# Performance work log

Measured on AMD Instinct MI355X. Metric: run time of the kernel, lower is better.

Reference implementation:

```python
import jax, jax.numpy as jnp
import numpy as np

H = 32        # num_attention_heads
KVH = 8       # num_key_value_heads
D = 64        # head_dim
HID = 2048    # hidden_size
G = H // KVH  # num_key_value_groups


def setup_inputs() -> dict:
    key = jax.random.key(0)
    k1, k2, k3, k4, k5 = jax.random.split(key, 5)
    B, S = 1, 2048
    s = 1.0 / np.sqrt(HID)
    return {
        "hidden_states": jax.random.normal(k1, (B, S, HID), dtype=jnp.float32),
        "attention_mask": jnp.ones((B, S), dtype=jnp.int32),
        "Wq": jax.random.normal(k2, (H * D, HID), dtype=jnp.float32) * s,
        "Wk": jax.random.normal(k3, (KVH * D, HID), dtype=jnp.float32) * s,
        "Wv": jax.random.normal(k4, (KVH * D, HID), dtype=jnp.float32) * s,
        "Wo": jax.random.normal(k5, (HID, HID), dtype=jnp.float32) * s,
    }


def reference(hidden_states, attention_mask, Wq, Wk, Wv, Wo):
    B, S, _ = hidden_states.shape
    dtype = hidden_states.dtype

    q = (hidden_states @ Wq.T).reshape(B, S, H, D).transpose(0, 2, 1, 3)     # [B,H,S,D]
    k = (hidden_states @ Wk.T).reshape(B, S, KVH, D).transpose(0, 2, 1, 3)   # [B,KVH,S,D]
    v = (hidden_states @ Wv.T).reshape(B, S, KVH, D).transpose(0, 2, 1, 3)

    # repeat_interleave over head dim: each KV head serves G query heads
    k = jnp.repeat(k, G, axis=1)  # [B,H,S,D]
    v = jnp.repeat(v, G, axis=1)

    scores = jnp.einsum('bhqd,bhkd->bhqk', q, k) / np.sqrt(D)  # [B,H,S,S]

    causal = jnp.tril(jnp.ones((S, S), dtype=dtype))                # [S,S]
    am = attention_mask.astype(dtype)[:, None, None, :]              # [B,1,1,S]
    mask = am * causal[None, None, :, :]                             # [B,1,S,S]
    mask = (1.0 - mask) * jnp.finfo(dtype).min
    scores = scores + mask                                           # broadcast over heads

    weights = jax.nn.softmax(scores, axis=-1)
    attn = jnp.einsum('bhqk,bhkd->bhqd', weights, v)                 # [B,H,S,D]
    attn = attn.transpose(0, 2, 1, 3).reshape(B, S, HID)
    return attn @ Wo.T
```

## Files before the change

kernel.cpp:

```cpp
#include <hip/hip_runtime.h>
#include <hip/hip_bf16.h>
#include <math.h>

typedef __attribute__((ext_vector_type(4))) float f32x4;
typedef __attribute__((ext_vector_type(16))) float f32x16;
typedef __attribute__((ext_vector_type(8))) short bf16x8;
typedef __attribute__((ext_vector_type(4))) short s16x4;
typedef __attribute__((ext_vector_type(4))) unsigned int u32x4;
typedef __attribute__((ext_vector_type(2))) unsigned int u32x2;
typedef short s16;
typedef unsigned int u32;
typedef unsigned short u16;

#define S_LEN 2048
#define HIDN  2048
#define QKVW  3072
#define NH    32
#define NKVH  8
#define HD    64

__device__ __forceinline__ s16 f2bf(float f) {
  unsigned int u = __float_as_uint(f);
  unsigned int lsb = (u >> 16) & 1u;
  u += 0x7fffu + lsb;
  return (s16)(u >> 16);
}

__device__ __forceinline__ u32 cvtpk(float lo, float hi) {
  u32 r;
  asm("v_cvt_pk_bf16_f32 %0, %1, %2" : "=v"(r) : "v"(lo), "v"(hi));
  return r;
}

__device__ __forceinline__ void gload16(const void* g, void* l) {
  __builtin_amdgcn_global_load_lds(
      (const __attribute__((address_space(1))) void*)g,
      (__attribute__((address_space(3))) void*)l, 16, 0, 0);
}

__device__ __forceinline__ void pls(u32& a, u32& b) {
  asm volatile("v_permlane32_swap_b32 %0, %1" : "+v"(a), "+v"(b));
}

__device__ __forceinline__ int swz7(int row) { return (row ^ (row >> 3)) & 7; }

__global__ __launch_bounds__(256) void cvt_all(const float* __restrict__ h,
                                               const float* __restrict__ wq,
                                               const float* __restrict__ wk,
                                               const float* __restrict__ wv,
                                               const float* __restrict__ wo,
                                               s16x4* __restrict__ dst) {
  int i = blockIdx.x * 256 + threadIdx.x;
  const float* src; int off;
  if (i < 1048576)      { src = h;  off = i; }
  else if (i < 2097152) { src = wq; off = i - 1048576; }
  else if (i < 2359296) { src = wk; off = i - 2097152; }
  else if (i < 2621440) { src = wv; off = i - 2359296; }
  else                  { src = wo; off = i - 2621440; }
  if (i < 3670016) {
    float4 f = reinterpret_cast<const float4*>(src)[off];
    s16x4 o;
    o.x = f2bf(f.x); o.y = f2bf(f.y); o.z = f2bf(f.z); o.w = f2bf(f.w);
    dst[i] = o;
  }
}

__device__ __forceinline__ void storeC(s16* C, size_t idx, float v)   { C[idx] = f2bf(v); }
__device__ __forceinline__ void storeC(float* C, size_t idx, float v) { C[idx] = v; }

template <typename OUT_T>
__global__ __launch_bounds__(512) void gemm_bt(const s16* __restrict__ A,
                                               const s16* __restrict__ B,
                                               OUT_T* __restrict__ C,
                                               int M, int N, int K, int gridX) {
  __shared__ alignas(16) s16 As[2][8192];
  __shared__ alignas(16) s16 Bs[2][8192];

  const int nwg  = (M >> 7) * gridX;
  const int flat = blockIdx.x;
  const int q8   = nwg >> 3;
  const int swz  = (flat & 7) * q8 + (flat >> 3);
  const int bm   = (swz / gridX) * 128;
  const int bn   = (swz % gridX) * 128;

  const int t    = threadIdx.x;
  const int lane = t & 63;
  const int w    = t >> 6;
  const int wr   = (w >> 2) * 64;
  const int wc   = (w & 3) * 32;
  const int lr   = lane & 15;
  const int lg   = lane >> 4;

  const int srow0 = (w * 2) * 8 + (lane >> 3);
  const int srow1 = (w * 2 + 1) * 8 + (lane >> 3);
  const int sl0   = ((lane & 7) ^ swz7(srow0)) * 8;
  const int sl1   = ((lane & 7) ^ swz7(srow1)) * 8;

  f32x4 acc[4][2];
#pragma unroll
  for (int m = 0; m < 4; ++m)
#pragma unroll
    for (int n = 0; n < 2; ++n)
      acc[m][n] = (f32x4){0.f, 0.f, 0.f, 0.f};

  const int nK = K >> 6;
  int buf = 0;

  {
    gload16(&A[(size_t)(bm + srow0) * K + sl0], (char*)As[0] + (w * 2) * 1024);
    gload16(&A[(size_t)(bm + srow1) * K + sl1], (char*)As[0] + (w * 2 + 1) * 1024);
    gload16(&B[(size_t)(bn + srow0) * K + sl0], (char*)Bs[0] + (w * 2) * 1024);
    gload16(&B[(size_t)(bn + srow1) * K + sl1], (char*)Bs[0] + (w * 2 + 1) * 1024);
  }
  __syncthreads();

  for (int ki = 0; ki < nK; ++ki) {
    if (ki + 1 < nK) {
      const int kt = (ki + 1) << 6;
      gload16(&A[(size_t)(bm + srow0) * K + kt + sl0], (char*)As[buf ^ 1] + (w * 2) * 1024);
      gload16(&A[(size_t)(bm + srow1) * K + kt + sl1], (char*)As[buf ^ 1] + (w * 2 + 1) * 1024);
      gload16(&B[(size_t)(bn + srow0) * K + kt + sl0], (char*)Bs[buf ^ 1] + (w * 2) * 1024);
      gload16(&B[(size_t)(bn + srow1) * K + kt + sl1], (char*)Bs[buf ^ 1] + (w * 2 + 1) * 1024);
    }

    bf16x8 af[4][2], bfr[2][2];
#pragma unroll
    for (int kk = 0; kk < 2; ++kk) {
#pragma unroll
      for (int m = 0; m < 4; ++m) {
        int row = wr + m * 16 + lr;
        af[m][kk] = *(bf16x8*)((char*)As[buf] + row * 128 + (((kk * 4 + lg) ^ swz7(row)) << 4));
      }
#pragma unroll
      for (int n = 0; n < 2; ++n) {
        int row = wc + n * 16 + lr;
        bfr[n][kk] = *(bf16x8*)((char*)Bs[buf] + row * 128 + (((kk * 4 + lg) ^ swz7(row)) << 4));
      }
    }

    __builtin_amdgcn_s_setprio(1);
#pragma unroll
    for (int m = 0; m < 4; ++m)
#pragma unroll
      for (int n = 0; n < 2; ++n)
#pragma unroll
        for (int kk = 0; kk < 2; ++kk)
          acc[m][n] = __builtin_amdgcn_mfma_f32_16x16x32_bf16(af[m][kk], bfr[n][kk], acc[m][n], 0, 0, 0);
    __builtin_amdgcn_s_setprio(0);

    __syncthreads();
    buf ^= 1;
  }

#pragma unroll
  for (int m = 0; m < 4; ++m)
#pragma unroll
    for (int n = 0; n < 2; ++n) {
      int row = bm + wr + m * 16 + lg * 4;
      int col = bn + wc + n * 16 + lr;
#pragma unroll
      for (int j = 0; j < 4; ++j)
        storeC(C, (size_t)(row + j) * N + col, acc[m][n][j]);
    }
}

__global__ __launch_bounds__(512) void attn_kernel(
    const s16* __restrict__ QKV,
    const int* __restrict__ am,
    s16* __restrict__ Ob) {
  __shared__ alignas(16) char smem[65536];
  __shared__ float2 mlb[4][64];

  const int t    = threadIdx.x;
  const int g    = t >> 8;
  const int tg   = t & 255;
  const int lane = t & 63;
  const int w    = tg >> 6;
  const int col  = lane & 31;
  const int hi   = lane >> 5;

  const int hk = blockIdx.x;
  const int p  = blockIdx.y;
  const int h  = hk * 4 + w;
  const int kbase = 2048 + hk * 64;
  const int vbase = 2560 + hk * 64;
  const float CF = 0.18033688f;

  const int krow   = lane >> 3;
  const int kslotb = lane & 7;
  const int vkv    = 2 * (tg >> 3);
  const int vd8    = (tg & 7) * 8;

  for (int phase = 0; phase < 2; ++phase) {
    const int qt = phase ? p : 63 - p;
    const int nt = (qt >> 1) + 1;
    const int R  = (nt + 1) >> 1;
    const int qrow = qt * 32 + col;

    bf16x8 qf[4];
#pragma unroll
    for (int ds = 0; ds < 4; ++ds)
      qf[ds] = *(const bf16x8*)&QKV[(size_t)qrow * QKVW + h * 64 + ds * 16 + hi * 8];

    if (g < nt) {
      char* Kn = smem + (g * 2 + 0) * 16384;
      char* Vn = Kn + 8192;
#pragma unroll
      for (int pp = 0; pp < 2; ++pp) {
        int c   = w * 2 + pp;
        int row = c * 8 + krow;
        int slot = kslotb ^ swz7(row);
        gload16(&QKV[(size_t)(g * 64 + row) * QKVW + kbase + slot * 8], Kn + c * 1024);
      }
      bf16x8 va = *(const bf16x8*)&QKV[(size_t)(g * 64 + vkv) * QKVW + vbase + vd8];
      bf16x8 vb = *(const bf16x8*)&QKV[(size_t)(g * 64 + vkv + 1) * QKVW + vbase + vd8];
#pragma unroll
      for (int i = 0; i < 8; ++i) {
        int d = vd8 + i;
        u32 pk = (u32)(u16)va[i] | ((u32)(u16)vb[i] << 16);
        *(u32*)&Vn[(d * 128 + vkv * 2) ^ (swz7(d) << 4)] = pk;
      }
    }
    int acur = am[g * 64 + lane];

    float m_i = -1e30f, l_part = 0.f;
    f32x16 Oacc[2];
#pragma unroll
    for (int b = 0; b < 2; ++b)
#pragma unroll
      for (int i = 0; i < 16; ++i) Oacc[b][i] = 0.f;
    __syncthreads();

    for (int it = 0; it < R; ++it) {
      const int buf  = it & 1;
      const int tile = 2 * it + g;
      const bool valid = (tile < nt);
      const int kv0  = tile * 64;
      const bool pre = (tile + 2 < nt);

      char* Kc = smem + (g * 2 + buf) * 16384;
      char* Vc = Kc + 8192;
      char* Kn = smem + (g * 2 + (buf ^ 1)) * 16384;
      char* Vn = Kn + 8192;

      bf16x8 va, vb;
      int anext = 0;
      if (pre) {
        const int nk0 = kv0 + 128;
#pragma unroll
        for (int pp = 0; pp < 2; ++pp) {
          int c   = w * 2 + pp;
          int row = c * 8 + krow;
          int slot = kslotb ^ swz7(row);
          gload16(&QKV[(size_t)(nk0 + row) * QKVW + kbase + slot * 8], Kn + c * 1024);
        }
        va = *(const bf16x8*)&QKV[(size_t)(nk0 + vkv) * QKVW + vbase + vd8];
        vb = *(const bf16x8*)&QKV[(size_t)(nk0 + vkv + 1) * QKVW + vbase + vd8];
        anext = am[nk0 + lane];
      }

      if (valid) {
        f32x16 s0, s1;
#pragma unroll
        for (int i = 0; i < 16; ++i) { s0[i] = 0.f; s1[i] = 0.f; }
        __builtin_amdgcn_s_setprio(1);
#pragma unroll
        for (int ds = 0; ds < 4; ++ds) {
          int off = ds * 32 + hi * 16;
          bf16x8 k0 = *(bf16x8*)&Kc[(col * 128 + off) ^ (swz7(col) << 4)];
          bf16x8 k1 = *(bf16x8*)&Kc[((32 + col) * 128 + off) ^ (swz7(32 + col) << 4)];
          s0 = __builtin_amdgcn_mfma_f32_32x32x16_bf16(k0, qf[ds], s0, 0, 0, 0);
          s1 = __builtin_amdgcn_mfma_f32_32x32x16_bf16(k1, qf[ds], s1, 0, 0, 0);
        }
        __builtin_amdgcn_s_setprio(0);

        float pvv[32];
        unsigned long long m64 = __ballot(acur != 0);
        bool interior = (kv0 + 64 <= qt * 32) && (m64 == ~0ull);
        if (interior) {
#pragma unroll
          for (int r = 0; r < 16; ++r) { pvv[r] = s0[r]; pvv[16 + r] = s1[r]; }
        } else {
#pragma unroll
          for (int b = 0; b < 2; ++b)
#pragma unroll
            for (int r = 0; r < 16; ++r) {
              int kvl = b * 32 + (r & 3) + 8 * (r >> 2) + 4 * hi;
              float sv = b ? s1[r] : s0[r];
              bool ok = (kv0 + kvl <= qrow) && ((m64 >> kvl) & 1ull);
              pvv[b * 16 + r] = ok ? sv : -INFINITY;
            }
        }

        float a0 = pvv[0], a1 = pvv[1], a2 = pvv[2], a3 = pvv[3];
#pragma unroll
        for (int i = 4; i < 32; i += 4) {
          a0 = fmaxf(a0, pvv[i]);     a1 = fmaxf(a1, pvv[i + 1]);
          a2 = fmaxf(a2, pvv[i + 2]); a3 = fmaxf(a3, pvv[i + 3]);
        }
        float lmax = fmaxf(fmaxf(a0, a1), fmaxf(a2, a3));
        lmax = fmaxf(lmax, __shfl_xor(lmax, 32));
        float lmaxs = lmax * CF;

        if (!__all(lmaxs - m_i <= 8.f)) {
          float nm = fmaxf(m_i, lmaxs);
          float al = __builtin_amdgcn_exp2f(m_i - nm);
          m_i = nm;
          l_part *= al;
#pragma unroll
          for (int b = 0; b < 2; ++b)
#pragma unroll
            for (int i = 0; i < 16; ++i) Oacc[b][i] *= al;
        }

        float t0 = 0.f, t1 = 0.f, t2 = 0.f, t3 = 0.f;
#pragma unroll
        for (int i = 0; i < 32; i += 4) {
          pvv[i]     = __builtin_amdgcn_exp2f(__builtin_fmaf(pvv[i],     CF, -m_i)); t0 += pvv[i];
          pvv[i + 1] = __builtin_amdgcn_exp2f(__builtin_fmaf(pvv[i + 1], CF, -m_i)); t1 += pvv[i + 1];
          pvv[i + 2] = __builtin_amdgcn_exp2f(__builtin_fmaf(pvv[i + 2], CF, -m_i)); t2 += pvv[i + 2];
          pvv[i + 3] = __builtin_amdgcn_exp2f(__builtin_fmaf(pvv[i + 3], CF, -m_i)); t3 += pvv[i + 3];
        }
        l_part += (t0 + t1) + (t2 + t3);

        bf16x8 pf[4];
#pragma unroll
        for (int b = 0; b < 2; ++b)
#pragma unroll
          for (int gg = 0; gg < 2; ++gg) {
            int base = b * 16 + gg * 8;
            u32 A1 = cvtpk(pvv[base + 0], pvv[base + 1]);
            u32 A2 = cvtpk(pvv[base + 2], pvv[base + 3]);
            u32 B1 = cvtpk(pvv[base + 4], pvv[base + 5]);
            u32 B2 = cvtpk(pvv[base + 6], pvv[base + 7]);
            pls(A1, B1);
            pls(A2, B2);
            u32x4 pw; pw[0] = A1; pw[1] = A2; pw[2] = B1; pw[3] = B2;
            pf[b * 2 + gg] = *reinterpret_cast<bf16x8*>(&pw);
          }

        __builtin_amdgcn_s_setprio(1);
#pragma unroll
        for (int ks = 0; ks < 4; ++ks) {
          int off = ks * 32 + hi * 16;
#pragma unroll
          for (int db = 0; db < 2; ++db) {
            int d = db * 32 + col;
            bf16x8 vf = *(bf16x8*)&Vc[(d * 128 + off) ^ (swz7(d) << 4)];
            Oacc[db] = __builtin_amdgcn_mfma_f32_32x32x16_bf16(vf, pf[ks], Oacc[db], 0, 0, 0);
          }
        }
        __builtin_amdgcn_s_setprio(0);
      }

      if (pre) {
#pragma unroll
        for (int i = 0; i < 8; ++i) {
          int d = vd8 + i;
          u32 pk = (u32)(u16)va[i] | ((u32)(u16)vb[i] << 16);
          *(u32*)&Vn[(d * 128 + vkv * 2) ^ (swz7(d) << 4)] = pk;
        }
        acur = anext;
      }
      __syncthreads();
    }

    float l_p = l_part + __shfl_xor(l_part, 32);

    if (g == 0) {
      float* pool = (float*)smem + w * 2048 + lane * 32;
#pragma unroll
      for (int b = 0; b < 2; ++b)
#pragma unroll
        for (int i = 0; i < 16; ++i) pool[b * 16 + i] = Oacc[b][i];
      mlb[w][lane] = make_float2(m_i, l_p);
    }
    __syncthreads();
    if (g == 1) {
      const float* pool = (const float*)smem + w * 2048 + lane * 32;
      float2 ml0 = mlb[w][lane];
      float mm = fmaxf(ml0.x, m_i);
      float b0 = __builtin_amdgcn_exp2f(ml0.x - mm);
      float b1 = __builtin_amdgcn_exp2f(m_i - mm);
      float linv = 1.0f / (ml0.y * b0 + l_p * b1);
      float sc0 = b0 * linv, sc1 = b1 * linv;
#pragma unroll
      for (int db = 0; db < 2; ++db)
#pragma unroll
        for (int qd = 0; qd < 4; ++qd) {
          float o0 = pool[db * 16 + qd * 4 + 0] * sc0 + Oacc[db][qd * 4 + 0] * sc1;
          float o1 = pool[db * 16 + qd * 4 + 1] * sc0 + Oacc[db][qd * 4 + 1] * sc1;
          float o2 = pool[db * 16 + qd * 4 + 2] * sc0 + Oacc[db][qd * 4 + 2] * sc1;
          float o3 = pool[db * 16 + qd * 4 + 3] * sc0 + Oacc[db][qd * 4 + 3] * sc1;
          u32x2 o;
          o[0] = cvtpk(o0, o1);
          o[1] = cvtpk(o2, o3);
          int d0 = db * 32 + qd * 8 + hi * 4;
          *(u32x2*)&Ob[(size_t)qrow * HIDN + h * 64 + d0] = o;
        }
    }
    __syncthreads();
  }
}

extern "C" void kernel_launch(void* const* d_in, const int* in_sizes, int n_in,
                              void* d_out, int out_size, void* d_ws, size_t ws_size,
                              hipStream_t stream) {
  const float* hidden = (const float*)d_in[0];
  const int*   am     = (const int*)d_in[1];
  const float* Wq     = (const float*)d_in[2];
  const float* Wk     = (const float*)d_in[3];
  const float* Wv     = (const float*)d_in[4];
  const float* Wo     = (const float*)d_in[5];
  float* out = (float*)d_out;

  s16* hb    = (s16*)d_ws;
  s16* wqkvb = hb    + 4194304;
  s16* wob   = wqkvb + 6291456;
  s16* QKVb  = wob   + 4194304;
  s16* Ab    = QKVb  + 6291456;

  cvt_all<<<14336, 256, 0, stream>>>(hidden, Wq, Wk, Wv, Wo, (s16x4*)d_ws);

  gemm_bt<s16><<<384, 512, 0, stream>>>(hb, wqkvb, QKVb, 2048, 3072, 2048, 24);

  attn_kernel<<<dim3(8, 32), 512, 0, stream>>>(QKVb, am, Ab);

  gemm_bt<float><<<256, 512, 0, stream>>>(Ab, wob, out, 2048, 2048, 2048, 16);
}
```

Before: 132.0 us.

## Split KV range across four warp-groups in attention with 4-way merge

The attention block grows from two to four 256-thread groups, each handling every fourth KV tile with its own double-buffered K/V shared memory, which doubles LDS to 128KB. Partial softmax states from three groups are merged by the fourth through swizzled f32x4 LDS stores. The aim is more parallelism per query tile and a shorter serial KV loop. In exchange, occupancy drops to one 1024-thread block per CU, and the merge adds extra LDS traffic plus a larger reduction.

```diff
diff --git a/kernel.cpp b/kernel.cpp
--- a/kernel.cpp
+++ b/kernel.cpp
@@ -164,12 +164,12 @@
     }
 }
 
-__global__ __launch_bounds__(512) void attn_kernel(
+__global__ __launch_bounds__(1024) void attn_kernel(
     const s16* __restrict__ QKV,
     const int* __restrict__ am,
     s16* __restrict__ Ob) {
-  __shared__ alignas(16) char smem[65536];
-  __shared__ float2 mlb[4][64];
+  __shared__ alignas(16) char smem[131072];
+  __shared__ float2 mlb[3][4][64];
 
   const int t    = threadIdx.x;
   const int g    = t >> 8;
@@ -190,11 +190,12 @@
   const int kslotb = lane & 7;
   const int vkv    = 2 * (tg >> 3);
   const int vd8    = (tg & 7) * 8;
+  const int psw    = lane & 7;
 
   for (int phase = 0; phase < 2; ++phase) {
     const int qt = phase ? p : 63 - p;
     const int nt = (qt >> 1) + 1;
-    const int R  = (nt + 1) >> 1;
+    const int R  = (nt + 3) >> 2;
     const int qrow = qt * 32 + col;
 
     bf16x8 qf[4];
@@ -203,7 +204,7 @@
       qf[ds] = *(const bf16x8*)&QKV[(size_t)qrow * QKVW + h * 64 + ds * 16 + hi * 8];
 
     if (g < nt) {
-      char* Kn = smem + (g * 2 + 0) * 16384;
+      char* Kn = smem + g * 32768;
       char* Vn = Kn + 8192;
 #pragma unroll
       for (int pp = 0; pp < 2; ++pp) {
@@ -233,20 +234,20 @@
 
     for (int it = 0; it < R; ++it) {
       const int buf  = it & 1;
-      const int tile = 2 * it + g;
+      const int tile = 4 * it + g;
       const bool valid = (tile < nt);
       const int kv0  = tile * 64;
-      const bool pre = (tile + 2 < nt);
-
-      char* Kc = smem + (g * 2 + buf) * 16384;
+      const bool pre = (tile + 4 < nt);
+
+      char* Kc = smem + g * 32768 + buf * 16384;
       char* Vc = Kc + 8192;
-      char* Kn = smem + (g * 2 + (buf ^ 1)) * 16384;
+      char* Kn = smem + g * 32768 + (buf ^ 1) * 16384;
       char* Vn = Kn + 8192;
 
       bf16x8 va, vb;
       int anext = 0;
       if (pre) {
-        const int nk0 = kv0 + 128;
+        const int nk0 = kv0 + 256;
 #pragma unroll
         for (int pp = 0; pp < 2; ++pp) {
           int c   = w * 2 + pp;
@@ -367,37 +368,47 @@
 
     float l_p = l_part + __shfl_xor(l_part, 32);
 
-    if (g == 0) {
-      float* pool = (float*)smem + w * 2048 + lane * 32;
-#pragma unroll
-      for (int b = 0; b < 2; ++b)
-#pragma unroll
-        for (int i = 0; i < 16; ++i) pool[b * 16 + i] = Oacc[b][i];
-      mlb[w][lane] = make_float2(m_i, l_p);
+    if (g < 3) {
+      float* pool = (float*)smem + g * 8192 + w * 2048 + lane * 32;
+#pragma unroll
+      for (int c = 0; c < 8; ++c) {
+        f32x4 v;
+#pragma unroll
+        for (int j = 0; j < 4; ++j) v[j] = Oacc[c >> 2][(c & 3) * 4 + j];
+        *(f32x4*)&pool[(c ^ psw) << 2] = v;
+      }
+      mlb[g][w][lane] = make_float2(m_i, l_p);
     }
     __syncthreads();
-    if (g == 1) {
-      const float* pool = (const float*)smem + w * 2048 + lane * 32;
-      float2 ml0 = mlb[w][lane];
-      float mm = fmaxf(ml0.x, m_i);
+    if (g == 3) {
+      const float* p0 = (float*)smem + 0 * 8192 + w * 2048 + lane * 32;
+      const float* p1 = (float*)smem + 1 * 8192 + w * 2048 + lane * 32;
+      const float* p2 = (float*)smem + 2 * 8192 + w * 2048 + lane * 32;
+      float2 ml0 = mlb[0][w][lane];
+      float2 ml1 = mlb[1][w][lane];
+      float2 ml2 = mlb[2][w][lane];
+      float mm = fmaxf(fmaxf(ml0.x, ml1.x), fmaxf(ml2.x, m_i));
       float b0 = __builtin_amdgcn_exp2f(ml0.x - mm);
-      float b1 = __builtin_amdgcn_exp2f(m_i - mm);
-      float linv = 1.0f / (ml0.y * b0 + l_p * b1);
-      float sc0 = b0 * linv, sc1 = b1 * linv;
-#pragma unroll
-      for (int db = 0; db < 2; ++db)
-#pragma unroll
-        for (int qd = 0; qd < 4; ++qd) {
-          float o0 = pool[db * 16 + qd * 4 + 0] * sc0 + Oacc[db][qd * 4 + 0] * sc1;
-          float o1 = pool[db * 16 + qd * 4 + 1] * sc0 + Oacc[db][qd * 4 + 1] * sc1;
-          float o2 = pool[db * 16 + qd * 4 + 2] * sc0 + Oacc[db][qd * 4 + 2] * sc1;
-          float o3 = pool[db * 16 + qd * 4 + 3] * sc0 + Oacc[db][qd * 4 + 3] * sc1;
-          u32x2 o;
-          o[0] = cvtpk(o0, o1);
-          o[1] = cvtpk(o2, o3);
-          int d0 = db * 32 + qd * 8 + hi * 4;
-          *(u32x2*)&Ob[(size_t)qrow * HIDN + h * 64 + d0] = o;
-        }
+      float b1 = __builtin_amdgcn_exp2f(ml1.x - mm);
+      float b2 = __builtin_amdgcn_exp2f(ml2.x - mm);
+      float b3 = __builtin_amdgcn_exp2f(m_i - mm);
+      float linv = 1.0f / (ml0.y * b0 + ml1.y * b1 + ml2.y * b2 + l_p * b3);
+      b0 *= linv; b1 *= linv; b2 *= linv; b3 *= linv;
+#pragma unroll
+      for (int c = 0; c < 8; ++c) {
+        f32x4 v0 = *(const f32x4*)&p0[(c ^ psw) << 2];
+        f32x4 v1 = *(const f32x4*)&p1[(c ^ psw) << 2];
+        f32x4 v2 = *(const f32x4*)&p2[(c ^ psw) << 2];
+        float o[4];
+#pragma unroll
+        for (int j = 0; j < 4; ++j)
+          o[j] = v0[j] * b0 + v1[j] * b1 + v2[j] * b2 + Oacc[c >> 2][(c & 3) * 4 + j] * b3;
+        u32x2 ov;
+        ov[0] = cvtpk(o[0], o[1]);
+        ov[1] = cvtpk(o[2], o[3]);
+        int d0 = (c >> 2) * 32 + (c & 3) * 8 + hi * 4;
+        *(u32x2*)&Ob[(size_t)qrow * HIDN + h * 64 + d0] = ov;
+      }
     }
     __syncthreads();
   }
@@ -424,7 +435,7 @@
 
   gemm_bt<s16><<<384, 512, 0, stream>>>(hb, wqkvb, QKVb, 2048, 3072, 2048, 24);
 
-  attn_kernel<<<dim3(8, 32), 512, 0, stream>>>(QKVb, am, Ab);
+  attn_kernel<<<dim3(8, 32), 1024, 0, stream>>>(QKVb, am, Ab);
 
   gemm_bt<float><<<256, 512, 0, stream>>>(Ab, wob, out, 2048, 2048, 2048, 16);
 }
```

After: 210.1 us. 59.2% more time.

## Process two KV tiles per iteration in attention with doubled LDS

Applied to the files above, without the earlier changes.

Each 256-thread group now handles two consecutive 64-row KV tiles per loop iteration instead of one. It computes both score blocks, takes one combined online-softmax max and rescale, and accumulates both PV products. The change halves the number of barriers, rescale checks and loop iterations, and doubles LDS to 128KB to hold double-buffered pairs of tiles. In exchange it raises register pressure and LDS use, which may reduce occupancy. Initial loads also fetch tiles unconditionally, relying on masking for tiles beyond the causal range.

```diff
diff --git a/kernel.cpp b/kernel.cpp
--- a/kernel.cpp
+++ b/kernel.cpp
@@ -11,6 +11,7 @@
 typedef short s16;
 typedef unsigned int u32;
 typedef unsigned short u16;
+typedef unsigned long long u64;
 
 #define S_LEN 2048
 #define HIDN  2048
@@ -168,7 +169,7 @@
     const s16* __restrict__ QKV,
     const int* __restrict__ am,
     s16* __restrict__ Ob) {
-  __shared__ alignas(16) char smem[65536];
+  __shared__ alignas(16) char smem[131072];
   __shared__ float2 mlb[4][64];
 
   const int t    = threadIdx.x;
@@ -191,10 +192,12 @@
   const int vkv    = 2 * (tg >> 3);
   const int vd8    = (tg & 7) * 8;
 
+  char* gbase = smem + g * 65536;
+
   for (int phase = 0; phase < 2; ++phase) {
     const int qt = phase ? p : 63 - p;
     const int nt = (qt >> 1) + 1;
-    const int R  = (nt + 1) >> 1;
+    const int R  = (nt + 3) >> 2;
     const int qrow = qt * 32 + col;
 
     bf16x8 qf[4];
@@ -202,64 +205,85 @@
     for (int ds = 0; ds < 4; ++ds)
       qf[ds] = *(const bf16x8*)&QKV[(size_t)qrow * QKVW + h * 64 + ds * 16 + hi * 8];
 
-    if (g < nt) {
-      char* Kn = smem + (g * 2 + 0) * 16384;
-      char* Vn = Kn + 8192;
-#pragma unroll
-      for (int pp = 0; pp < 2; ++pp) {
-        int c   = w * 2 + pp;
-        int row = c * 8 + krow;
-        int slot = kslotb ^ swz7(row);
-        gload16(&QKV[(size_t)(g * 64 + row) * QKVW + kbase + slot * 8], Kn + c * 1024);
-      }
-      bf16x8 va = *(const bf16x8*)&QKV[(size_t)(g * 64 + vkv) * QKVW + vbase + vd8];
-      bf16x8 vb = *(const bf16x8*)&QKV[(size_t)(g * 64 + vkv + 1) * QKVW + vbase + vd8];
-#pragma unroll
-      for (int i = 0; i < 8; ++i) {
-        int d = vd8 + i;
-        u32 pk = (u32)(u16)va[i] | ((u32)(u16)vb[i] << 16);
-        *(u32*)&Vn[(d * 128 + vkv * 2) ^ (swz7(d) << 4)] = pk;
-      }
-    }
-    int acur = am[g * 64 + lane];
-
-    float m_i = -1e30f, l_part = 0.f;
-    f32x16 Oacc[2];
-#pragma unroll
-    for (int b = 0; b < 2; ++b)
-#pragma unroll
-      for (int i = 0; i < 16; ++i) Oacc[b][i] = 0.f;
-    __syncthreads();
-
-    for (int it = 0; it < R; ++it) {
-      const int buf  = it & 1;
-      const int tile = 2 * it + g;
-      const bool valid = (tile < nt);
-      const int kv0  = tile * 64;
-      const bool pre = (tile + 2 < nt);
-
-      char* Kc = smem + (g * 2 + buf) * 16384;
-      char* Vc = Kc + 8192;
-      char* Kn = smem + (g * 2 + (buf ^ 1)) * 16384;
-      char* Vn = Kn + 8192;
-
-      bf16x8 va, vb;
-      int anext = 0;
-      if (pre) {
-        const int nk0 = kv0 + 128;
+    {
+#pragma unroll
+      for (int sub = 0; sub < 2; ++sub) {
+        const int tt = 2 * g + sub;
+        char* Kd = gbase + sub * 16384;
+        char* Vd = Kd + 8192;
 #pragma unroll
         for (int pp = 0; pp < 2; ++pp) {
           int c   = w * 2 + pp;
           int row = c * 8 + krow;
           int slot = kslotb ^ swz7(row);
-          gload16(&QKV[(size_t)(nk0 + row) * QKVW + kbase + slot * 8], Kn + c * 1024);
-        }
-        va = *(const bf16x8*)&QKV[(size_t)(nk0 + vkv) * QKVW + vbase + vd8];
-        vb = *(const bf16x8*)&QKV[(size_t)(nk0 + vkv + 1) * QKVW + vbase + vd8];
-        anext = am[nk0 + lane];
-      }
-
-      if (valid) {
+          gload16(&QKV[(size_t)(tt * 64 + row) * QKVW + kbase + slot * 8], Kd + c * 1024);
+        }
+        bf16x8 va = *(const bf16x8*)&QKV[(size_t)(tt * 64 + vkv) * QKVW + vbase + vd8];
+        bf16x8 vb = *(const bf16x8*)&QKV[(size_t)(tt * 64 + vkv + 1) * QKVW + vbase + vd8];
+#pragma unroll
+        for (int i = 0; i < 8; ++i) {
+          int d = vd8 + i;
+          u32 pk = (u32)(u16)va[i] | ((u32)(u16)vb[i] << 16);
+          *(u32*)&Vd[(d * 128 + vkv * 2) ^ (swz7(d) << 4)] = pk;
+        }
+      }
+    }
+    int a0 = am[2 * g * 64 + lane];
+    int a1 = am[2 * g * 64 + 64 + lane];
+
+    float m_i = -1e30f, l_part = 0.f;
+    f32x16 Oacc[2];
+#pragma unroll
+    for (int b = 0; b < 2; ++b)
+#pragma unroll
+      for (int i = 0; i < 16; ++i) Oacc[b][i] = 0.f;
+    __syncthreads();
+
+    for (int it = 0; it < R; ++it) {
+      const int buf = it & 1;
+      const int t0  = 4 * it + 2 * g;
+      const int kv0 = t0 * 64;
+      const bool v0 = (t0 < nt);
+      const bool v1 = (t0 + 1 < nt);
+
+      char* Kc0 = gbase + buf * 32768;
+      char* Vc0 = Kc0 + 8192;
+      char* Kc1 = Kc0 + 16384;
+      char* Vc1 = Kc0 + 24576;
+      char* Kn  = gbase + (buf ^ 1) * 32768;
+
+      bf16x8 va0, vb0, va1, vb1;
+      int an0 = 0, an1 = 0;
+      const bool p0 = (t0 + 4 < nt), p1 = (t0 + 5 < nt);
+      if (p0) {
+        const int nk = kv0 + 256;
+#pragma unroll
+        for (int pp = 0; pp < 2; ++pp) {
+          int c   = w * 2 + pp;
+          int row = c * 8 + krow;
+          int slot = kslotb ^ swz7(row);
+          gload16(&QKV[(size_t)(nk + row) * QKVW + kbase + slot * 8], Kn + c * 1024);
+        }
+        va0 = *(const bf16x8*)&QKV[(size_t)(nk + vkv) * QKVW + vbase + vd8];
+        vb0 = *(const bf16x8*)&QKV[(size_t)(nk + vkv + 1) * QKVW + vbase + vd8];
+        an0 = am[nk + lane];
+      }
+      if (p1) {
+        const int nk = kv0 + 320;
+#pragma unroll
+        for (int pp = 0; pp < 2; ++pp) {
+          int c   = w * 2 + pp;
+          int row = c * 8 + krow;
+          int slot = kslotb ^ swz7(row);
+          gload16(&QKV[(size_t)(nk + row) * QKVW + kbase + slot * 8], Kn + 16384 + c * 1024);
+        }
+        va1 = *(const bf16x8*)&QKV[(size_t)(nk + vkv) * QKVW + vbase + vd8];
+        vb1 = *(const bf16x8*)&QKV[(size_t)(nk + vkv + 1) * QKVW + vbase + vd8];
+        an1 = am[nk + lane];
+      }
+
+      float pvA[32], pvB[32];
+      {
         f32x16 s0, s1;
 #pragma unroll
         for (int i = 0; i < 16; ++i) { s0[i] = 0.f; s1[i] = 0.f; }
@@ -267,19 +291,17 @@
 #pragma unroll
         for (int ds = 0; ds < 4; ++ds) {
           int off = ds * 32 + hi * 16;
-          bf16x8 k0 = *(bf16x8*)&Kc[(col * 128 + off) ^ (swz7(col) << 4)];
-          bf16x8 k1 = *(bf16x8*)&Kc[((32 + col) * 128 + off) ^ (swz7(32 + col) << 4)];
+          bf16x8 k0 = *(bf16x8*)&Kc0[(col * 128 + off) ^ (swz7(col) << 4)];
+          bf16x8 k1 = *(bf16x8*)&Kc0[((32 + col) * 128 + off) ^ (swz7(32 + col) << 4)];
           s0 = __builtin_amdgcn_mfma_f32_32x32x16_bf16(k0, qf[ds], s0, 0, 0, 0);
           s1 = __builtin_amdgcn_mfma_f32_32x32x16_bf16(k1, qf[ds], s1, 0, 0, 0);
         }
         __builtin_amdgcn_s_setprio(0);
-
-        float pvv[32];
-        unsigned long long m64 = __ballot(acur != 0);
-        bool interior = (kv0 + 64 <= qt * 32) && (m64 == ~0ull);
-        if (interior) {
-#pragma unroll
-          for (int r = 0; r < 16; ++r) { pvv[r] = s0[r]; pvv[16 + r] = s1[r]; }
+        u64 m64 = __ballot(a0 != 0);
+        bool inter = v0 && (kv0 + 64 <= qt * 32) && (m64 == ~0ull);
+        if (inter) {
+#pragma unroll
+          for (int r = 0; r < 16; ++r) { pvA[r] = s0[r]; pvA[16 + r] = s1[r]; }
         } else {
 #pragma unroll
           for (int b = 0; b < 2; ++b)
@@ -287,80 +309,142 @@
             for (int r = 0; r < 16; ++r) {
               int kvl = b * 32 + (r & 3) + 8 * (r >> 2) + 4 * hi;
               float sv = b ? s1[r] : s0[r];
-              bool ok = (kv0 + kvl <= qrow) && ((m64 >> kvl) & 1ull);
-              pvv[b * 16 + r] = ok ? sv : -INFINITY;
+              bool ok = v0 && (kv0 + kvl <= qrow) && ((m64 >> kvl) & 1ull);
+              pvA[b * 16 + r] = ok ? sv : -INFINITY;
             }
         }
-
-        float a0 = pvv[0], a1 = pvv[1], a2 = pvv[2], a3 = pvv[3];
-#pragma unroll
-        for (int i = 4; i < 32; i += 4) {
-          a0 = fmaxf(a0, pvv[i]);     a1 = fmaxf(a1, pvv[i + 1]);
-          a2 = fmaxf(a2, pvv[i + 2]); a3 = fmaxf(a3, pvv[i + 3]);
-        }
-        float lmax = fmaxf(fmaxf(a0, a1), fmaxf(a2, a3));
-        lmax = fmaxf(lmax, __shfl_xor(lmax, 32));
-        float lmaxs = lmax * CF;
-
-        if (!__all(lmaxs - m_i <= 8.f)) {
-          float nm = fmaxf(m_i, lmaxs);
-          float al = __builtin_amdgcn_exp2f(m_i - nm);
-          m_i = nm;
-          l_part *= al;
+      }
+      {
+        f32x16 s0, s1;
+#pragma unroll
+        for (int i = 0; i < 16; ++i) { s0[i] = 0.f; s1[i] = 0.f; }
+        __builtin_amdgcn_s_setprio(1);
+#pragma unroll
+        for (int ds = 0; ds < 4; ++ds) {
+          int off = ds * 32 + hi * 16;
+          bf16x8 k0 = *(bf16x8*)&Kc1[(col * 128 + off) ^ (swz7(col) << 4)];
+          bf16x8 k1 = *(bf16x8*)&Kc1[((32 + col) * 128 + off) ^ (swz7(32 + col) << 4)];
+          s0 = __builtin_amdgcn_mfma_f32_32x32x16_bf16(k0, qf[ds], s0, 0, 0, 0);
+          s1 = __builtin_amdgcn_mfma_f32_32x32x16_bf16(k1, qf[ds], s1, 0, 0, 0);
+        }
+        __builtin_amdgcn_s_setprio(0);
+        u64 m64 = __ballot(a1 != 0);
+        const int kvb = kv0 + 64;
+        bool inter = v1 && (kvb + 64 <= qt * 32) && (m64 == ~0ull);
+        if (inter) {
+#pragma unroll
+          for (int r = 0; r < 16; ++r) { pvB[r] = s0[r]; pvB[16 + r] = s1[r]; }
+        } else {
 #pragma unroll
           for (int b = 0; b < 2; ++b)
 #pragma unroll
-            for (int i = 0; i < 16; ++i) Oacc[b][i] *= al;
-        }
-
-        float t0 = 0.f, t1 = 0.f, t2 = 0.f, t3 = 0.f;
-#pragma unroll
-        for (int i = 0; i < 32; i += 4) {
-          pvv[i]     = __builtin_amdgcn_exp2f(__builtin_fmaf(pvv[i],     CF, -m_i)); t0 += pvv[i];
-          pvv[i + 1] = __builtin_amdgcn_exp2f(__builtin_fmaf(pvv[i + 1], CF, -m_i)); t1 += pvv[i + 1];
-          pvv[i + 2] = __builtin_amdgcn_exp2f(__builtin_fmaf(pvv[i + 2], CF, -m_i)); t2 += pvv[i + 2];
-          pvv[i + 3] = __builtin_amdgcn_exp2f(__builtin_fmaf(pvv[i + 3], CF, -m_i)); t3 += pvv[i + 3];
-        }
-        l_part += (t0 + t1) + (t2 + t3);
-
-        bf16x8 pf[4];
+            for (int r = 0; r < 16; ++r) {
+              int kvl = b * 32 + (r & 3) + 8 * (r >> 2) + 4 * hi;
+              float sv = b ? s1[r] : s0[r];
+              bool ok = v1 && (kvb + kvl <= qrow) && ((m64 >> kvl) & 1ull);
+              pvB[b * 16 + r] = ok ? sv : -INFINITY;
+            }
+        }
+      }
+
+      float a0t = fmaxf(pvA[0], pvB[0]), a1t = fmaxf(pvA[1], pvB[1]);
+      float a2t = fmaxf(pvA[2], pvB[2]), a3t = fmaxf(pvA[3], pvB[3]);
+#pragma unroll
+      for (int i = 4; i < 32; i += 4) {
+        a0t = fmaxf(a0t, fmaxf(pvA[i],     pvB[i]));
+        a1t = fmaxf(a1t, fmaxf(pvA[i + 1], pvB[i + 1]));
+        a2t = fmaxf(a2t, fmaxf(pvA[i + 2], pvB[i + 2]));
+        a3t = fmaxf(a3t, fmaxf(pvA[i + 3], pvB[i + 3]));
+      }
+      float lmax = fmaxf(fmaxf(a0t, a1t), fmaxf(a2t, a3t));
+      lmax = fmaxf(lmax, __shfl_xor(lmax, 32));
+      float lmaxs = lmax * CF;
+
+      if (!__all(lmaxs - m_i <= 8.f)) {
+        float nm = fmaxf(m_i, lmaxs);
+        float al = __builtin_amdgcn_exp2f(m_i - nm);
+        m_i = nm;
+        l_part *= al;
 #pragma unroll
         for (int b = 0; b < 2; ++b)
 #pragma unroll
-          for (int gg = 0; gg < 2; ++gg) {
-            int base = b * 16 + gg * 8;
-            u32 A1 = cvtpk(pvv[base + 0], pvv[base + 1]);
-            u32 A2 = cvtpk(pvv[base + 2], pvv[base + 3]);
-            u32 B1 = cvtpk(pvv[base + 4], pvv[base + 5]);
-            u32 B2 = cvtpk(pvv[base + 6], pvv[base + 7]);
-            pls(A1, B1);
-            pls(A2, B2);
-            u32x4 pw; pw[0] = A1; pw[1] = A2; pw[2] = B1; pw[3] = B2;
-            pf[b * 2 + gg] = *reinterpret_cast<bf16x8*>(&pw);
-          }
-
-        __builtin_amdgcn_s_setprio(1);
-#pragma unroll
-        for (int ks = 0; ks < 4; ++ks) {
-          int off = ks * 32 + hi * 16;
-#pragma unroll
-          for (int db = 0; db < 2; ++db) {
-            int d = db * 32 + col;
-            bf16x8 vf = *(bf16x8*)&Vc[(d * 128 + off) ^ (swz7(d) << 4)];
-            Oacc[db] = __builtin_amdgcn_mfma_f32_32x32x16_bf16(vf, pf[ks], Oacc[db], 0, 0, 0);
-          }
-        }
-        __builtin_amdgcn_s_setprio(0);
-      }
-
-      if (pre) {
+          for (int i = 0; i < 16; ++i) Oacc[b][i] *= al;
+      }
+
+      float s0t = 0.f, s1t = 0.f, s2t = 0.f, s3t = 0.f;
+#pragma unroll
+      for (int i = 0; i < 32; i += 4) {
+        pvA[i]     = __builtin_amdgcn_exp2f(__builtin_fmaf(pvA[i],     CF, -m_i)); s0t += pvA[i];
+        pvA[i + 1] = __builtin_amdgcn_exp2f(__builtin_fmaf(pvA[i + 1], CF, -m_i)); s1t += pvA[i + 1];
+        pvA[i + 2] = __builtin_amdgcn_exp2f(__builtin_fmaf(pvA[i + 2], CF, -m_i)); s2t += pvA[i + 2];
+        pvA[i + 3] = __builtin_amdgcn_exp2f(__builtin_fmaf(pvA[i + 3], CF, -m_i)); s3t += pvA[i + 3];
+      }
+#pragma unroll
+      for (int i = 0; i < 32; i += 4) {
+        pvB[i]     = __builtin_amdgcn_exp2f(__builtin_fmaf(pvB[i],     CF, -m_i)); s0t += pvB[i];
+        pvB[i + 1] = __builtin_amdgcn_exp2f(__builtin_fmaf(pvB[i + 1], CF, -m_i)); s1t += pvB[i + 1];
+        pvB[i + 2] = __builtin_amdgcn_exp2f(__builtin_fmaf(pvB[i + 2], CF, -m_i)); s2t += pvB[i + 2];
+        pvB[i + 3] = __builtin_amdgcn_exp2f(__builtin_fmaf(pvB[i + 3], CF, -m_i)); s3t += pvB[i + 3];
+      }
+      l_part += (s0t + s1t) + (s2t + s3t);
+
+      bf16x8 pfA[4], pfB[4];
+#pragma unroll
+      for (int b = 0; b < 2; ++b)
+#pragma unroll
+        for (int gg = 0; gg < 2; ++gg) {
+          int base = b * 16 + gg * 8;
+          u32 A1 = cvtpk(pvA[base + 0], pvA[base + 1]);
+          u32 A2 = cvtpk(pvA[base + 2], pvA[base + 3]);
+          u32 B1 = cvtpk(pvA[base + 4], pvA[base + 5]);
+          u32 B2 = cvtpk(pvA[base + 6], pvA[base + 7]);
+          pls(A1, B1); pls(A2, B2);
+          u32x4 pw; pw[0] = A1; pw[1] = A2; pw[2] = B1; pw[3] = B2;
+          pfA[b * 2 + gg] = *reinterpret_cast<bf16x8*>(&pw);
+          u32 C1 = cvtpk(pvB[base + 0], pvB[base + 1]);
+          u32 C2 = cvtpk(pvB[base + 2], pvB[base + 3]);
+          u32 D1 = cvtpk(pvB[base + 4], pvB[base + 5]);
+          u32 D2 = cvtpk(pvB[base + 6], pvB[base + 7]);
+          pls(C1, D1); pls(C2, D2);
+          u32x4 qw; qw[0] = C1; qw[1] = C2; qw[2] = D1; qw[3] = D2;
+          pfB[b * 2 + gg] = *reinterpret_cast<bf16x8*>(&qw);
+        }
+
+      __builtin_amdgcn_s_setprio(1);
+#pragma unroll
+      for (int ks = 0; ks < 4; ++ks) {
+        int off = ks * 32 + hi * 16;
+#pragma unroll
+        for (int db = 0; db < 2; ++db) {
+          int d = db * 32 + col;
+          int sw = swz7(d) << 4;
+          bf16x8 vfA = *(bf16x8*)&Vc0[(d * 128 + off) ^ sw];
+          Oacc[db] = __builtin_amdgcn_mfma_f32_32x32x16_bf16(vfA, pfA[ks], Oacc[db], 0, 0, 0);
+          bf16x8 vfB = *(bf16x8*)&Vc1[(d * 128 + off) ^ sw];
+          Oacc[db] = __builtin_amdgcn_mfma_f32_32x32x16_bf16(vfB, pfB[ks], Oacc[db], 0, 0, 0);
+        }
+      }
+      __builtin_amdgcn_s_setprio(0);
+
+      if (p0) {
+        char* Vn = Kn + 8192;
 #pragma unroll
         for (int i = 0; i < 8; ++i) {
           int d = vd8 + i;
-          u32 pk = (u32)(u16)va[i] | ((u32)(u16)vb[i] << 16);
+          u32 pk = (u32)(u16)va0[i] | ((u32)(u16)vb0[i] << 16);
           *(u32*)&Vn[(d * 128 + vkv * 2) ^ (swz7(d) << 4)] = pk;
         }
-        acur = anext;
+        a0 = an0;
+      }
+      if (p1) {
+        char* Vn = Kn + 24576;
+#pragma unroll
+        for (int i = 0; i < 8; ++i) {
+          int d = vd8 + i;
+          u32 pk = (u32)(u16)va1[i] | ((u32)(u16)vb1[i] << 16);
+          *(u32*)&Vn[(d * 128 + vkv * 2) ^ (swz7(d) << 4)] = pk;
+        }
+        a1 = an1;
       }
       __syncthreads();
     }
```

Result: slower. 150.3 us (+13.9%).
